# Kernel optimization log

Hardware: AMD Instinct MI355X
Metric: run time of the kernel (lower is better)

## Reference

```python
import jax, jax.numpy as jnp
import numpy as np

N = 262144   # query points
M = 131072   # gather-source points
C = 256      # c1 == c2
H = C // 8   # gating bottleneck
EPS = 1e-5


def _bn(x, g, b):
    # BatchNorm1d in training mode: biased batch stats over the point dim.
    mu = jnp.mean(x, axis=0)
    var = jnp.mean((x - mu) ** 2, axis=0)
    return (x - mu) * jax.lax.rsqrt(var + EPS) * g + b


def setup_inputs() -> dict:
    key = jax.random.key(0)
    ks = jax.random.split(key, 8)
    p = jax.random.normal(ks[0], (N, 3), dtype=jnp.float32)
    x = jax.random.normal(ks[1], (N, C), dtype=jnp.float32)
    gx = jax.random.normal(ks[2], (M, C), dtype=jnp.float32)
    idx = jax.random.randint(ks[3], (N,), 0, M, dtype=jnp.int64)
    s = 0.05
    return {
        "p": p, "x": x, "gx": gx, "idx": idx,
        # nn.Linear(c1, c1, bias=False)
        "Wlin": jax.random.normal(ks[4], (C, C), dtype=jnp.float32) * s,
        # self.bn
        "g_main": jnp.ones((C,), jnp.float32), "b_main": jnp.zeros((C,), jnp.float32),
        # linear_w: BN(c2) -> Linear(c2, c2//8) -> BN(c2//8) -> Linear(c2//8, c2)
        "g_a": jnp.ones((C,), jnp.float32), "b_a": jnp.zeros((C,), jnp.float32),
        "W1": jax.random.normal(ks[5], (H, C), dtype=jnp.float32) * s,
        "b1": jnp.zeros((H,), jnp.float32),
        "g_b": jnp.ones((H,), jnp.float32), "b_b": jnp.zeros((H,), jnp.float32),
        "W2": jax.random.normal(ks[6], (C, H), dtype=jnp.float32) * s,
        "b2": jnp.zeros((C,), jnp.float32),
    }


def reference(p, x, gx, idx, Wlin, g_main, b_main, g_a, b_a, W1, b1, g_b, b_b, W2, b2):
    # kNN(k=1) gather: aug_feat = gx[idx]
    aug = gx[idx]                                    # (N, C)
    # relation '-' with c1 == c2
    rel = x - aug                                    # (N, C)
    # linear_w gating MLP
    rel = jax.nn.relu(_bn(rel, g_a, b_a))
    rel = rel @ W1.T + b1                            # (N, H)
    rel = jax.nn.relu(_bn(rel, g_b, b_b))
    rel = rel @ W2.T + b2                            # (N, C)
    sw = jax.nn.softmax(rel, axis=1)
    # residual combine (c1 == c2 branch), then Linear -> BN -> ReLU
    x2 = x + sw * aug                                # (N, C)
    out = jax.nn.relu(_bn(x2 @ Wlin.T, g_main, b_main))
    return out  # p, o are passed through unchanged by the module
```

## Files before the change

kernel.cpp:

```cpp
#include <hip/hip_runtime.h>
#include <stdint.h>
#include <stddef.h>

#define N_PTS 262144
#define M_PTS 131072
#define C_DIM 256
#define H_DIM 32
#define EPS_BN 1e-5f
#define NSLOT_A 64
#define NSLOT_B 16
#define NSLOT_T 64

using s16x8 = __attribute__((ext_vector_type(8))) short;
using s16x4 = __attribute__((ext_vector_type(4))) short;
using f32x4 = __attribute__((ext_vector_type(4))) float;

__device__ __forceinline__ short f2bf(float f) {
  __bf16 h = (__bf16)f;
  return __builtin_bit_cast(short, h);
}
__device__ __forceinline__ float bf2f(short s) {
  unsigned int u = ((unsigned int)(unsigned short)s) << 16;
  return __builtin_bit_cast(float, u);
}
__device__ __forceinline__ f32x4 mfma16(s16x8 a, s16x8 b, f32x4 c) {
  return __builtin_amdgcn_mfma_f32_16x16x32_bf16(a, b, c, 0, 0, 0);
}

__global__ __launch_bounds__(256) void k_prep(
    const float* __restrict__ W1, const float* __restrict__ W2,
    const float* __restrict__ Wlin, short* __restrict__ W1b,
    short* __restrict__ W2b, short* __restrict__ Wlb2) {
  int i = blockIdx.x * 256 + threadIdx.x;
  if (i < 8192) {
    W1b[i] = f2bf(W1[i]);
  } else if (i < 16384) {
    W2b[i - 8192] = f2bf(W2[i - 8192]);
  } else {
    int s = i - 16384;
    int col = s >> 8, k = s & 255;
    int ksl = k >> 5, kg = (k >> 3) & 3, e = k & 7;
    int n = col >> 4, cl = col & 15;
    Wlb2[ksl * 8192 + n * 512 + kg * 128 + cl * 8 + e] = f2bf(Wlin[s]);
  }
}

__global__ __launch_bounds__(256) void k_rel(
    const float* __restrict__ x, const float* __restrict__ gx,
    const int* __restrict__ idx, short* __restrict__ rel,
    float* __restrict__ sum_a) {
  __shared__ float red[4][512];
  int t = threadIdx.x;
  int w = t >> 6;
  int c4 = (t & 63) * 4;
  int r0 = blockIdx.x * 128;
  float s0 = 0, s1 = 0, s2 = 0, s3 = 0, q0 = 0, q1 = 0, q2 = 0, q3 = 0;
#pragma unroll 4
  for (int it = 0; it < 32; ++it) {
    int r = r0 + it * 4 + w;
    int ir = idx[r];
    float4 xv = *(const float4*)(x + (size_t)r * 256 + c4);
    float4 gv = *(const float4*)(gx + (size_t)ir * 256 + c4);
    float d0 = xv.x - gv.x, d1 = xv.y - gv.y, d2 = xv.z - gv.z, d3 = xv.w - gv.w;
    s16x4 h;
    h[0] = f2bf(d0); h[1] = f2bf(d1); h[2] = f2bf(d2); h[3] = f2bf(d3);
    *(s16x4*)(rel + (size_t)r * 256 + c4) = h;
    s0 += d0; s1 += d1; s2 += d2; s3 += d3;
    q0 += d0 * d0; q1 += d1 * d1; q2 += d2 * d2; q3 += d3 * d3;
  }
  red[w][c4 + 0] = s0; red[w][c4 + 1] = s1; red[w][c4 + 2] = s2; red[w][c4 + 3] = s3;
  red[w][256 + c4 + 0] = q0; red[w][256 + c4 + 1] = q1;
  red[w][256 + c4 + 2] = q2; red[w][256 + c4 + 3] = q3;
  __syncthreads();
  float vs = red[0][t] + red[1][t] + red[2][t] + red[3][t];
  float vq = red[0][256 + t] + red[1][256 + t] + red[2][256 + t] + red[3][256 + t];
  float* slot = sum_a + (size_t)(blockIdx.x & (NSLOT_A - 1)) * 512;
  atomicAdd(&slot[t], vs);
  atomicAdd(&slot[256 + t], vq);
}

__global__ void k_fin(const float* __restrict__ sums, const float* __restrict__ g,
                      const float* __restrict__ b, float* __restrict__ sc,
                      float* __restrict__ sh, int n, float invN, int nslot) {
  int c = threadIdx.x;
  if (c < n) {
    float S = 0.f, Q = 0.f;
    for (int s = 0; s < nslot; ++s) {
      S += sums[(size_t)s * 2 * n + c];
      Q += sums[(size_t)s * 2 * n + n + c];
    }
    float mu = S * invN;
    float var = Q * invN - mu * mu;
    float rs = rsqrtf(var + EPS_BN);
    float scale = g[c] * rs;
    sc[c] = scale;
    sh[c] = b[c] - mu * scale;
  }
}

__global__ __launch_bounds__(256) void k_y(
    const short* __restrict__ rel, const short* __restrict__ W1b,
    const float* __restrict__ sc_a, const float* __restrict__ sh_a,
    short* __restrict__ yh, float* __restrict__ sum_b) {
  __shared__ __attribute__((aligned(16))) short Ab[64 * 264];
  __shared__ float lsc[256];
  __shared__ float lsh[256];
  __shared__ float red[4][64];
  int t = threadIdx.x;
  lsc[t] = sc_a[t];
  lsh[t] = sh_a[t];
  {
    int srow = t >> 2, sseg = (t & 3) * 64;
    const short* src = rel + (size_t)(blockIdx.x * 64 + srow) * 256 + sseg;
    short* dst = Ab + srow * 264 + sseg;
#pragma unroll
    for (int j = 0; j < 8; ++j)
      *(s16x8*)(dst + j * 8) = *(const s16x8*)(src + j * 8);
  }
  __syncthreads();
  int w = t >> 6, l = t & 63, l15 = l & 15, kg = l >> 4;
  int r0 = blockIdx.x * 64 + w * 16;
  const short* arow = Ab + (w * 16 + l15) * 264;

  s16x8 bfr[2][8];
#pragma unroll
  for (int j = 0; j < 2; ++j)
#pragma unroll
    for (int kk = 0; kk < 8; ++kk)
      bfr[j][kk] = *(const s16x8*)(W1b + (j * 16 + l15) * 256 + kg * 8 + kk * 32);

  f32x4 acc0 = {0.f, 0.f, 0.f, 0.f};
  f32x4 acc1 = {0.f, 0.f, 0.f, 0.f};
#pragma unroll
  for (int kk = 0; kk < 8; ++kk) {
    int k0 = kg * 8 + kk * 32;
    s16x8 a = *(const s16x8*)(arow + k0);
    s16x8 af;
#pragma unroll
    for (int i = 0; i < 8; ++i) {
      float v = bf2f(a[i]);
      v = fmaxf(v * lsc[k0 + i] + lsh[k0 + i], 0.f);
      af[i] = f2bf(v);
    }
    acc0 = mfma16(af, bfr[0][kk], acc0);
    acc1 = mfma16(af, bfr[1][kk], acc1);
  }

  float s0 = 0.f, q0 = 0.f, s1 = 0.f, q1 = 0.f;
#pragma unroll
  for (int reg = 0; reg < 4; ++reg) {
    int gr = r0 + kg * 4 + reg;
    float y0 = acc0[reg], y1 = acc1[reg];
    yh[(size_t)gr * 32 + l15] = f2bf(y0);
    yh[(size_t)gr * 32 + 16 + l15] = f2bf(y1);
    s0 += y0; q0 += y0 * y0;
    s1 += y1; q1 += y1 * y1;
  }
  s0 += __shfl_xor(s0, 16); s0 += __shfl_xor(s0, 32);
  q0 += __shfl_xor(q0, 16); q0 += __shfl_xor(q0, 32);
  s1 += __shfl_xor(s1, 16); s1 += __shfl_xor(s1, 32);
  q1 += __shfl_xor(q1, 16); q1 += __shfl_xor(q1, 32);
  if (l < 16) {
    red[w][l15] = s0;
    red[w][16 + l15] = s1;
    red[w][32 + l15] = q0;
    red[w][48 + l15] = q1;
  }
  __syncthreads();
  if (t < 64) {
    float v = red[0][t] + red[1][t] + red[2][t] + red[3][t];
    atomicAdd(&sum_b[(size_t)(blockIdx.x & (NSLOT_B - 1)) * 64 + t], v);
  }
}

__global__ __launch_bounds__(256) void k_x2g(
    const short* __restrict__ yh, const short* __restrict__ W2b,
    const float* __restrict__ b2, const float* __restrict__ x,
    const short* __restrict__ Wlb2, const float* __restrict__ sc_b,
    const float* __restrict__ sh_b, short* __restrict__ big,
    float* __restrict__ sum_t) {
  __shared__ __attribute__((aligned(16))) short swl[64 * 264];
  __shared__ __attribute__((aligned(16))) short bb[8192];
  __shared__ float ls[512];
  int t = threadIdx.x, w = t >> 6, l = t & 63, l15 = l & 15, kg = l >> 4;
  int r0 = blockIdx.x * 64 + w * 16;
  int lr = r0 + l15;

  s16x8 yb = *(const s16x8*)(yh + (size_t)lr * 32 + kg * 8);
  s16x8 af;
#pragma unroll
  for (int i = 0; i < 8; ++i) {
    int k = kg * 8 + i;
    float v = bf2f(yb[i]);
    v = fmaxf(v * sc_b[k] + sh_b[k], 0.f);
    af[i] = f2bf(v);
  }
  f32x4 zero = {0.f, 0.f, 0.f, 0.f};
  f32x4 z[16];
#pragma unroll
  for (int n = 0; n < 16; ++n) {
    s16x8 bf = *(const s16x8*)(W2b + (n * 16 + l15) * 32 + kg * 8);
    z[n] = mfma16(af, bf, zero);
  }
  float b2c[16];
#pragma unroll
  for (int n = 0; n < 16; ++n) b2c[n] = b2[n * 16 + l15];
  float mx[4] = {-3.4e38f, -3.4e38f, -3.4e38f, -3.4e38f};
#pragma unroll
  for (int n = 0; n < 16; ++n)
#pragma unroll
    for (int r = 0; r < 4; ++r) {
      z[n][r] += b2c[n];
      mx[r] = fmaxf(mx[r], z[n][r]);
    }
#pragma unroll
  for (int r = 0; r < 4; ++r) {
    mx[r] = fmaxf(mx[r], __shfl_xor(mx[r], 1));
    mx[r] = fmaxf(mx[r], __shfl_xor(mx[r], 2));
    mx[r] = fmaxf(mx[r], __shfl_xor(mx[r], 4));
    mx[r] = fmaxf(mx[r], __shfl_xor(mx[r], 8));
  }
  float sm[4] = {0.f, 0.f, 0.f, 0.f};
#pragma unroll
  for (int n = 0; n < 16; ++n)
#pragma unroll
    for (int r = 0; r < 4; ++r) {
      float e = __expf(z[n][r] - mx[r]);
      z[n][r] = e;
      sm[r] += e;
    }
#pragma unroll
  for (int r = 0; r < 4; ++r) {
    sm[r] += __shfl_xor(sm[r], 1);
    sm[r] += __shfl_xor(sm[r], 2);
    sm[r] += __shfl_xor(sm[r], 4);
    sm[r] += __shfl_xor(sm[r], 8);
    sm[r] = 1.f / sm[r];
  }
#pragma unroll
  for (int n = 0; n < 16; ++n)
#pragma unroll
    for (int r = 0; r < 4; ++r)
      swl[(w * 16 + kg * 4 + r) * 264 + n * 16 + l15] = f2bf(z[n][r] * sm[r]);
  __syncthreads();

  int brow0 = blockIdx.x * 64;
  int c4 = (t & 63) * 4;
#pragma unroll 4
  for (int it = 0; it < 16; ++it) {
    int row = it * 4 + w;
    size_t goff = (size_t)(brow0 + row) * 256 + c4;
    float4 xv = *(const float4*)(x + goff);
    s16x4 rv = *(const s16x4*)(big + goff);
    s16x4 sv = *(const s16x4*)(swl + row * 264 + c4);
    s16x4 h;
#pragma unroll
    for (int j = 0; j < 4; ++j) {
      float xf = xv[j];
      float aug = xf - bf2f(rv[j]);
      h[j] = f2bf(xf + bf2f(sv[j]) * aug);
    }
    *(s16x4*)(swl + row * 264 + c4) = h;
  }
  __syncthreads();

  f32x4 acc[16];
#pragma unroll
  for (int n = 0; n < 16; ++n) acc[n] = zero;
#pragma unroll 1
  for (int ksl = 0; ksl < 8; ++ksl) {
    if (ksl) __syncthreads();
    {
      const short* src = Wlb2 + (size_t)ksl * 8192;
#pragma unroll
      for (int j = 0; j < 4; ++j)
        *(s16x8*)(bb + j * 2048 + t * 8) = *(const s16x8*)(src + j * 2048 + t * 8);
    }
    __syncthreads();
    s16x8 a = *(const s16x8*)(swl + (w * 16 + l15) * 264 + ksl * 32 + kg * 8);
#pragma unroll
    for (int n = 0; n < 16; ++n) {
      s16x8 b = *(const s16x8*)(bb + (n * 64 + l) * 8);
      acc[n] = mfma16(a, b, acc[n]);
    }
  }

  ls[t] = 0.f;
  ls[256 + t] = 0.f;
  __syncthreads();
#pragma unroll
  for (int n = 0; n < 16; ++n) {
    float sY = acc[n][0] + acc[n][1] + acc[n][2] + acc[n][3];
    float sQ = acc[n][0] * acc[n][0] + acc[n][1] * acc[n][1] +
               acc[n][2] * acc[n][2] + acc[n][3] * acc[n][3];
    sY += __shfl_xor(sY, 16); sY += __shfl_xor(sY, 32);
    sQ += __shfl_xor(sQ, 16); sQ += __shfl_xor(sQ, 32);
    if (l < 16) {
      atomicAdd(&ls[n * 16 + l15], sY);
      atomicAdd(&ls[256 + n * 16 + l15], sQ);
    }
  }
  __syncthreads();
  float* slot = sum_t + (size_t)(blockIdx.x & (NSLOT_T - 1)) * 512;
  atomicAdd(&slot[t], ls[t]);
  atomicAdd(&slot[256 + t], ls[256 + t]);

#pragma unroll
  for (int n = 0; n < 16; ++n) {
#pragma unroll
    for (int r = 0; r < 4; ++r) {
      int gr = brow0 + w * 16 + kg * 4 + r;
      big[(size_t)gr * 256 + n * 16 + l15] = f2bf(acc[n][r]);
    }
  }
}

__global__ __launch_bounds__(256) void k_out(
    const short* __restrict__ tbuf, const float* __restrict__ sc_m,
    const float* __restrict__ sh_m, float* __restrict__ out) {
  __shared__ float lsc[256];
  __shared__ float lsh[256];
  int t = threadIdx.x;
  lsc[t] = sc_m[t];
  lsh[t] = sh_m[t];
  __syncthreads();
  int u0 = blockIdx.x * 256 + t;
#pragma unroll 2
  for (int it = 0; it < 8; ++it) {
    int u = u0 + it * (2048 * 256);
    int c16 = (u & 15) * 16;
    s16x8 tv0 = *(const s16x8*)(tbuf + (size_t)u * 16);
    s16x8 tv1 = *(const s16x8*)(tbuf + (size_t)u * 16 + 8);
    float4 o[4];
#pragma unroll
    for (int q = 0; q < 4; ++q) {
      float4 sc = *(const float4*)(lsc + c16 + q * 4);
      float4 sh = *(const float4*)(lsh + c16 + q * 4);
      short e0 = (q < 2) ? tv0[(q & 1) * 4 + 0] : tv1[(q & 1) * 4 + 0];
      short e1 = (q < 2) ? tv0[(q & 1) * 4 + 1] : tv1[(q & 1) * 4 + 1];
      short e2 = (q < 2) ? tv0[(q & 1) * 4 + 2] : tv1[(q & 1) * 4 + 2];
      short e3 = (q < 2) ? tv0[(q & 1) * 4 + 3] : tv1[(q & 1) * 4 + 3];
      o[q].x = fmaxf(bf2f(e0) * sc.x + sh.x, 0.f);
      o[q].y = fmaxf(bf2f(e1) * sc.y + sh.y, 0.f);
      o[q].z = fmaxf(bf2f(e2) * sc.z + sh.z, 0.f);
      o[q].w = fmaxf(bf2f(e3) * sc.w + sh.w, 0.f);
    }
#pragma unroll
    for (int q = 0; q < 4; ++q)
      *(float4*)(out + (size_t)u * 16 + q * 4) = o[q];
  }
}

extern "C" void kernel_launch(void* const* d_in, const int* in_sizes, int n_in,
                              void* d_out, int out_size, void* d_ws, size_t ws_size,
                              hipStream_t stream) {
  const float* x      = (const float*)d_in[1];
  const float* gx     = (const float*)d_in[2];
  const int*   idx    = (const int*)d_in[3];
  const float* Wlin   = (const float*)d_in[4];
  const float* g_main = (const float*)d_in[5];
  const float* b_main = (const float*)d_in[6];
  const float* g_a    = (const float*)d_in[7];
  const float* b_a    = (const float*)d_in[8];
  const float* W1     = (const float*)d_in[9];
  const float* g_b    = (const float*)d_in[11];
  const float* b_b    = (const float*)d_in[12];
  const float* W2     = (const float*)d_in[13];
  const float* b2     = (const float*)d_in[14];
  float* out = (float*)d_out;
  float* wsf = (float*)d_ws;

  float* sum_b = wsf;
  float* sc_a = wsf + 1024; float* sh_a = wsf + 1280;
  float* sc_b = wsf + 1536; float* sh_b = wsf + 1568;
  float* sc_m = wsf + 1600; float* sh_m = wsf + 1856;
  short* W1b  = (short*)(wsf + 2112);
  short* W2b  = (short*)(wsf + 6208);
  short* Wlb2 = (short*)(wsf + 10304);

  size_t big_off = (ws_size - (size_t)134217728) & ~(size_t)1023;
  size_t yh_off  = big_off - (size_t)16777216;
  short* big = (short*)((char*)d_ws + big_off);
  short* yh  = (short*)((char*)d_ws + yh_off);

  float* sum_t = out + (size_t)N_PTS * 256 - 65536;
  float* sum_a = out + (size_t)N_PTS * 256 - 32768;

  hipMemsetAsync(sum_b, 0, 1024 * sizeof(float), stream);
  hipMemsetAsync(sum_t, 0, 65536 * sizeof(float), stream);
  k_prep<<<320, 256, 0, stream>>>(W1, W2, Wlin, W1b, W2b, Wlb2);
  k_rel<<<N_PTS / 128, 256, 0, stream>>>(x, gx, idx, big, sum_a);
  k_fin<<<1, 256, 0, stream>>>(sum_a, g_a, b_a, sc_a, sh_a, 256, 1.f / N_PTS, NSLOT_A);
  k_y<<<N_PTS / 64, 256, 0, stream>>>(big, W1b, sc_a, sh_a, yh, sum_b);
  k_fin<<<1, 64, 0, stream>>>(sum_b, g_b, b_b, sc_b, sh_b, 32, 1.f / N_PTS, NSLOT_B);
  k_x2g<<<N_PTS / 64, 256, 0, stream>>>(yh, W2b, b2, x, Wlb2, sc_b, sh_b, big, sum_t);
  k_fin<<<1, 256, 0, stream>>>(sum_t, g_main, b_main, sc_m, sh_m, 256, 1.f / N_PTS, NSLOT_T);
  k_out<<<2048, 256, 0, stream>>>(big, sc_m, sh_m, out);
}
```

Baseline: 522.4 us.

## Split final GEMM by output columns per wave with register-prefetched weights

The final Wlin GEMM in k_x2g changes how work is split across waves. Each wave now owns 64 output columns across all 64 rows, not 16 rows across all columns. Each wave loads its weight fragments straight from global memory into registers and double-buffers them one k-slice ahead. This removes the LDS staging buffer and the two barriers per k-slice. Because each wave now owns distinct columns, the shared-memory atomics used for the BN statistics are replaced by plain stores. The cost is more global weight traffic per block (served from L2) and more A-fragment reads from LDS.

```diff
diff --git a/kernel.cpp b/kernel.cpp
--- a/kernel.cpp
+++ b/kernel.cpp
@@ -180,7 +180,6 @@
     const float* __restrict__ sh_b, short* __restrict__ big,
     float* __restrict__ sum_t) {
   __shared__ __attribute__((aligned(16))) short swl[64 * 264];
-  __shared__ __attribute__((aligned(16))) short bb[8192];
   __shared__ float ls[512];
   int t = threadIdx.x, w = t >> 6, l = t & 63, l15 = l & 15, kg = l >> 4;
   int r0 = blockIdx.x * 64 + w * 16;
@@ -243,6 +242,11 @@
     for (int r = 0; r < 4; ++r)
       swl[(w * 16 + kg * 4 + r) * 264 + n * 16 + l15] = f2bf(z[n][r] * sm[r]);
   __syncthreads();
+
+  s16x8 bf0[4], bf1[4];
+#pragma unroll
+  for (int np = 0; np < 4; ++np)
+    bf0[np] = *(const s16x8*)(Wlb2 + (w * 4 + np) * 512 + l * 8);
 
   int brow0 = blockIdx.x * 64;
   int c4 = (t & 63) * 4;
@@ -267,37 +271,40 @@
   f32x4 acc[16];
 #pragma unroll
   for (int n = 0; n < 16; ++n) acc[n] = zero;
-#pragma unroll 1
+#pragma unroll
   for (int ksl = 0; ksl < 8; ++ksl) {
-    if (ksl) __syncthreads();
-    {
-      const short* src = Wlb2 + (size_t)ksl * 8192;
-#pragma unroll
-      for (int j = 0; j < 4; ++j)
-        *(s16x8*)(bb + j * 2048 + t * 8) = *(const s16x8*)(src + j * 2048 + t * 8);
-    }
-    __syncthreads();
-    s16x8 a = *(const s16x8*)(swl + (w * 16 + l15) * 264 + ksl * 32 + kg * 8);
-#pragma unroll
-    for (int n = 0; n < 16; ++n) {
-      s16x8 b = *(const s16x8*)(bb + (n * 64 + l) * 8);
-      acc[n] = mfma16(a, b, acc[n]);
-    }
-  }
-
-  ls[t] = 0.f;
-  ls[256 + t] = 0.f;
-  __syncthreads();
-#pragma unroll
-  for (int n = 0; n < 16; ++n) {
-    float sY = acc[n][0] + acc[n][1] + acc[n][2] + acc[n][3];
-    float sQ = acc[n][0] * acc[n][0] + acc[n][1] * acc[n][1] +
-               acc[n][2] * acc[n][2] + acc[n][3] * acc[n][3];
+    if (ksl < 7) {
+#pragma unroll
+      for (int np = 0; np < 4; ++np)
+        bf1[np] = *(const s16x8*)(Wlb2 + (size_t)(ksl + 1) * 8192 + (w * 4 + np) * 512 + l * 8);
+    }
+#pragma unroll
+    for (int rg = 0; rg < 4; ++rg) {
+      s16x8 a = *(const s16x8*)(swl + (rg * 16 + l15) * 264 + ksl * 32 + kg * 8);
+#pragma unroll
+      for (int np = 0; np < 4; ++np)
+        acc[rg * 4 + np] = mfma16(a, bf0[np], acc[rg * 4 + np]);
+    }
+#pragma unroll
+    for (int np = 0; np < 4; ++np) bf0[np] = bf1[np];
+  }
+
+#pragma unroll
+  for (int np = 0; np < 4; ++np) {
+    float sY = 0.f, sQ = 0.f;
+#pragma unroll
+    for (int rg = 0; rg < 4; ++rg)
+#pragma unroll
+      for (int r = 0; r < 4; ++r) {
+        float v = acc[rg * 4 + np][r];
+        sY += v;
+        sQ += v * v;
+      }
     sY += __shfl_xor(sY, 16); sY += __shfl_xor(sY, 32);
     sQ += __shfl_xor(sQ, 16); sQ += __shfl_xor(sQ, 32);
     if (l < 16) {
-      atomicAdd(&ls[n * 16 + l15], sY);
-      atomicAdd(&ls[256 + n * 16 + l15], sQ);
+      ls[(w * 4 + np) * 16 + l15] = sY;
+      ls[256 + (w * 4 + np) * 16 + l15] = sQ;
     }
   }
   __syncthreads();
@@ -306,13 +313,14 @@
   atomicAdd(&slot[256 + t], ls[256 + t]);
 
 #pragma unroll
-  for (int n = 0; n < 16; ++n) {
+  for (int rg = 0; rg < 4; ++rg)
 #pragma unroll
     for (int r = 0; r < 4; ++r) {
-      int gr = brow0 + w * 16 + kg * 4 + r;
-      big[(size_t)gr * 256 + n * 16 + l15] = f2bf(acc[n][r]);
-    }
-  }
+      int gr = brow0 + rg * 16 + kg * 4 + r;
+#pragma unroll
+      for (int np = 0; np < 4; ++np)
+        big[(size_t)gr * 256 + (w * 4 + np) * 16 + l15] = f2bf(acc[rg * 4 + np][r]);
+    }
 }
 
 __global__ __launch_bounds__(256) void k_out(
```

Result: faster. 490.5 us (-6.1%).
